# Performance work log

Hardware: AMD Instinct MI355X
Metric: run time of the kernel (lower is better)

Reference implementation:

```python
import jax, jax.numpy as jnp
import numpy as np
import math

RADIUS = 32
NUM_HEADS = 8

B, L, DIM = 2, 8192, 256


def setup_inputs() -> dict:
    key = jax.random.key(0)
    k1, k2, k3, k4, k5 = jax.random.split(key, 5)
    s_in = 1.0 / math.sqrt(DIM)
    return {
        "x": jax.random.normal(k1, (B, L, DIM), dtype=jnp.float32),
        "w_qkv": jax.random.normal(k2, (DIM, 3 * DIM), dtype=jnp.float32) * s_in,
        "b_qkv": jax.random.normal(k3, (3 * DIM,), dtype=jnp.float32) * 0.01,
        "w_proj": jax.random.normal(k4, (DIM, DIM), dtype=jnp.float32) * s_in,
        "b_proj": jax.random.normal(k5, (DIM,), dtype=jnp.float32) * 0.01,
    }


def reference(x, w_qkv, b_qkv, w_proj, b_proj):
    B, L, dim = x.shape
    H = NUM_HEADS
    hd = dim // H
    R = RADIUS
    W = 2 * R + 1
    scale = math.sqrt(hd)

    qkv = x @ w_qkv + b_qkv                      # (B, L, 3*dim)
    qkv = qkv.reshape(B, L, 3, H, hd)
    qkv = jnp.transpose(qkv, (2, 0, 3, 1, 4))    # (3, B, H, L, hd)
    q = qkv[0].reshape(B * H, L, hd)
    k = qkv[1].reshape(B * H, L, hd)
    v = qkv[2].reshape(B * H, L, hd)

    # zero-pad along sequence (matches F.pad value=0: boundary windows attend
    # to zero vectors with logit 0, included in softmax)
    k_p = jnp.pad(k, ((0, 0), (R, R), (0, 0)))   # (BH, L+2R, hd)
    v_p = jnp.pad(v, ((0, 0), (R, R), (0, 0)))

    idx = jnp.arange(L)[:, None] + jnp.arange(W)[None, :]  # (L, W)
    k_w = k_p[:, idx]                            # (BH, L, W, hd)
    v_w = v_p[:, idx]                            # (BH, L, W, hd)

    scores = jnp.einsum('bld,blwd->blw', q, k_w) / scale
    attn = jax.nn.softmax(scores, axis=-1)
    out = jnp.einsum('blw,blwd->bld', attn, v_w)  # (BH, L, hd)

    out = out.reshape(B, H, L, hd)
    out = jnp.transpose(out, (0, 2, 1, 3)).reshape(B, L, dim)
    return out @ w_proj + b_proj
```

## Files before the change

kernel.cpp:

```cpp
#include <hip/hip_runtime.h>
#include <hip/hip_bf16.h>
#include <math.h>

#define B_SZ 2
#define L_SZ 8192
#define DIM 256
#define H_N 8
#define HD 32
#define RAD 32
#define M_ROWS (B_SZ * L_SZ)

typedef __bf16 bf16x8 __attribute__((ext_vector_type(8)));
typedef __bf16 bf16x4 __attribute__((ext_vector_type(4)));
typedef short  s16x4  __attribute__((ext_vector_type(4)));
typedef float  f32x4  __attribute__((ext_vector_type(4)));

typedef const __attribute__((address_space(1))) void gvoid_t;
typedef __attribute__((address_space(3))) void lvoid_t;

static __device__ __forceinline__ f32x4 mfma16_bf16(bf16x4 a, bf16x4 b, f32x4 c) {
#if __has_builtin(__builtin_amdgcn_mfma_f32_16x16x16bf16_1k)
    return __builtin_amdgcn_mfma_f32_16x16x16bf16_1k(
        __builtin_bit_cast(s16x4, a), __builtin_bit_cast(s16x4, b), c, 0, 0, 0);
#elif __has_builtin(__builtin_amdgcn_mfma_f32_16x16x16_bf16)
    return __builtin_amdgcn_mfma_f32_16x16x16_bf16(a, b, c, 0, 0, 0);
#else
    f32x4 d = c;
    asm volatile("v_mfma_f32_16x16x16_bf16 %0, %1, %2, %0\n\ts_nop 7\n\ts_nop 7"
                 : "+v"(d) : "v"(a), "v"(b));
    return d;
#endif
}

__global__ __launch_bounds__(256) void prep(const float* __restrict__ wq,
                                            const float* __restrict__ wp,
                                            __bf16* __restrict__ wqT,
                                            __bf16* __restrict__ wpT) {
    int idx = blockIdx.x * 256 + threadIdx.x;
    const int N2 = 3 * DIM * DIM;
    if (idx < N2) {
        int n = idx >> 8, k = idx & 255;
        wqT[idx] = (__bf16)wq[(size_t)k * (3 * DIM) + n];
    } else {
        int i3 = idx - N2;
        int n = i3 >> 8, k = i3 & 255;
        wpT[i3] = (__bf16)wp[(size_t)k * DIM + n];
    }
}

template<int BM, int BN, int WM, int WN, int N_DIM, int K_DIM, bool OUT_BF16, bool CAST_A>
__global__ __launch_bounds__(256) void gemm_bt(const void* __restrict__ Aptr,
                                               const __bf16* __restrict__ BT,
                                               const float* __restrict__ bias,
                                               void* __restrict__ Cout) {
    constexpr int BK = 32;
    constexpr int FM = BM / WM / 16;
    constexpr int FN = BN / WN / 16;
    __shared__ __bf16 As[BM * BK];
    __shared__ __bf16 Bs[BN * BK];
    const int tid = threadIdx.x;
    const int lane = tid & 63;
    const int wave = tid >> 6;
    const int wr = wave / WN;
    const int wc = wave % WN;
    const int row0 = blockIdx.y * BM;
    const int col0 = blockIdx.x * BN;

    f32x4 acc[FM][FN] = {};

    const int fr = lane & 15;
    const int fg = lane >> 4;

    for (int k0 = 0; k0 < K_DIM; k0 += BK) {
        #pragma unroll
        for (int i = 0; i < BN / 64; ++i) {
            int c  = tid + i * 256;
            int r  = c >> 2;
            int kk = (c & 3) * 8;
            __builtin_amdgcn_global_load_lds(
                (gvoid_t*)(BT + (size_t)(col0 + r) * K_DIM + (k0 + kk)),
                (lvoid_t*)(Bs + c * 8), 16, 0, 0);
        }
        if (CAST_A) {
            const float* Af = (const float*)Aptr;
            #pragma unroll
            for (int i = 0; i < BM / 64; ++i) {
                int c  = tid + i * 256;
                int r  = c >> 2;
                int kk = (c & 3) * 8;
                const float* ap = Af + (size_t)(row0 + r) * K_DIM + (k0 + kk);
                float4 v0 = *reinterpret_cast<const float4*>(ap);
                float4 v1 = *reinterpret_cast<const float4*>(ap + 4);
                bf16x8 w;
                w[0] = (__bf16)v0.x; w[1] = (__bf16)v0.y; w[2] = (__bf16)v0.z; w[3] = (__bf16)v0.w;
                w[4] = (__bf16)v1.x; w[5] = (__bf16)v1.y; w[6] = (__bf16)v1.z; w[7] = (__bf16)v1.w;
                *reinterpret_cast<bf16x8*>(As + c * 8) = w;
            }
        } else {
            const __bf16* Ab = (const __bf16*)Aptr;
            #pragma unroll
            for (int i = 0; i < BM / 64; ++i) {
                int c  = tid + i * 256;
                int r  = c >> 2;
                int kk = (c & 3) * 8;
                __builtin_amdgcn_global_load_lds(
                    (gvoid_t*)(Ab + (size_t)(row0 + r) * K_DIM + (k0 + kk)),
                    (lvoid_t*)(As + c * 8), 16, 0, 0);
            }
        }
        asm volatile("s_waitcnt vmcnt(0)" ::: "memory");
        __syncthreads();

        bf16x8 a[FM], b[FN];
        #pragma unroll
        for (int i = 0; i < FM; ++i)
            a[i] = *reinterpret_cast<const bf16x8*>(&As[(wr * (BM / WM) + i * 16 + fr) * BK + fg * 8]);
        #pragma unroll
        for (int j = 0; j < FN; ++j)
            b[j] = *reinterpret_cast<const bf16x8*>(&Bs[(wc * (BN / WN) + j * 16 + fr) * BK + fg * 8]);
        #pragma unroll
        for (int i = 0; i < FM; ++i)
            #pragma unroll
            for (int j = 0; j < FN; ++j)
                acc[i][j] = __builtin_amdgcn_mfma_f32_16x16x32_bf16(a[i], b[j], acc[i][j], 0, 0, 0);
        __syncthreads();
    }

    #pragma unroll
    for (int i = 0; i < FM; ++i) {
        #pragma unroll
        for (int j = 0; j < FN; ++j) {
            int cc = col0 + wc * (BN / WN) + j * 16 + fr;
            float bv = bias[cc];
            #pragma unroll
            for (int r = 0; r < 4; ++r) {
                int rr = row0 + wr * (BM / WM) + i * 16 + fg * 4 + r;
                float v = acc[i][j][r] + bv;
                if (OUT_BF16)
                    ((__bf16*)Cout)[(size_t)rr * N_DIM + cc] = (__bf16)v;
                else
                    ((float*)Cout)[(size_t)rr * N_DIM + cc] = v;
            }
        }
    }
}

__global__ __launch_bounds__(256) void natt_mfma(const __bf16* __restrict__ qkv,
                                                 __bf16* __restrict__ attn_out) {
    constexpr int VS = 216;
    __shared__ __bf16 vsT[32 * VS];

    const int tid  = threadIdx.x;
    const int lane = tid & 63;
    const int wave = tid >> 6;
    const int l15  = lane & 15;
    const int fg   = lane >> 4;
    const int bh = blockIdx.y;
    const int b  = bh >> 3;
    const int h  = bh & 7;
    const int bq0 = blockIdx.x * 128;
    const int wq0 = bq0 + wave * 32;

    const __bf16* base = qkv + (size_t)b * L_SZ * 768 + h * 32;

    #pragma unroll
    for (int i = 0; i < 3; ++i) {
        int c  = tid + i * 256;
        int sp = c >> 2;
        int dq = c & 3;
        int kp = bq0 - 32 + sp;
        bf16x8 v = {};
        if (kp >= 0 && kp < L_SZ)
            v = *reinterpret_cast<const bf16x8*>(base + (size_t)kp * 768 + 512 + dq * 8);
        int g = (sp >> 3) ^ dq;
        #pragma unroll
        for (int j = 0; j < 8; ++j)
            vsT[(dq * 8 + j) * VS + g * 8 + (sp & 7)] = v[j];
    }

    bf16x8 kf[6];
    #pragma unroll
    for (int t = 0; t < 6; ++t) {
        int kp = wq0 - 32 + t * 16 + l15;
        bf16x8 kv = {};
        if (kp >= 0 && kp < L_SZ)
            kv = *reinterpret_cast<const bf16x8*>(base + (size_t)kp * 768 + 256 + fg * 8);
        kf[t] = kv;
    }
    bf16x8 qf[2];
    #pragma unroll
    for (int s = 0; s < 2; ++s)
        qf[s] = *reinterpret_cast<const bf16x8*>(base + (size_t)(wq0 + s * 16 + l15) * 768 + fg * 8);

    __syncthreads();

    const float rscale = 0.17677669529663687f;

    #pragma unroll
    for (int s = 0; s < 2; ++s) {
        f32x4 st[5];
        __builtin_amdgcn_s_setprio(1);
        #pragma unroll
        for (int t = 0; t < 5; ++t)
            st[t] = __builtin_amdgcn_mfma_f32_16x16x32_bf16(kf[s + t], qf[s], f32x4{}, 0, 0, 0);
        __builtin_amdgcn_s_setprio(0);

        const int qr = l15;
        float sum = 0.f;
        #pragma unroll
        for (int t = 0; t < 5; ++t) {
            #pragma unroll
            for (int r = 0; r < 4; ++r) {
                int pr = 16 * t + 4 * fg + r;
                bool valid = (pr >= qr) && (pr <= qr + 64);
                float e = valid ? __expf(st[t][r] * rscale) : 0.f;
                st[t][r] = e;
                sum += e;
            }
        }
        sum += __shfl_xor(sum, 16);
        sum += __shfl_xor(sum, 32);
        float inv = 1.f / sum;

        bf16x4 pf[5];
        #pragma unroll
        for (int t = 0; t < 5; ++t) {
            bf16x4 p;
            #pragma unroll
            for (int r = 0; r < 4; ++r) p[r] = (__bf16)(st[t][r] * inv);
            pf[t] = p;
        }

        f32x4 acc[2] = {};
        __builtin_amdgcn_s_setprio(1);
        #pragma unroll
        for (int c = 0; c < 5; ++c) {
            #pragma unroll
            for (int dt = 0; dt < 2; ++dt) {
                int g = (4 * wave + 2 * s + 2 * c + (fg >> 1)) ^ (2 * dt + (l15 >> 3));
                bf16x4 vf = *reinterpret_cast<const bf16x4*>(
                    &vsT[(dt * 16 + l15) * VS + g * 8 + 4 * (fg & 1)]);
                acc[dt] = mfma16_bf16(pf[c], vf, acc[dt]);
            }
        }
        __builtin_amdgcn_s_setprio(0);

        __bf16* outp = attn_out + ((size_t)(b * L_SZ + wq0 + s * 16)) * 256 + h * 32;
        #pragma unroll
        for (int dt = 0; dt < 2; ++dt)
            #pragma unroll
            for (int r = 0; r < 4; ++r)
                outp[(size_t)(fg * 4 + r) * 256 + dt * 16 + l15] = (__bf16)acc[dt][r];
    }
}

extern "C" void kernel_launch(void* const* d_in, const int* in_sizes, int n_in,
                              void* d_out, int out_size, void* d_ws, size_t ws_size,
                              hipStream_t stream) {
    const float* x      = (const float*)d_in[0];
    const float* w_qkv  = (const float*)d_in[1];
    const float* b_qkv  = (const float*)d_in[2];
    const float* w_proj = (const float*)d_in[3];
    const float* b_proj = (const float*)d_in[4];
    float* out = (float*)d_out;

    __bf16* wqkvT  = (__bf16*)d_ws;
    __bf16* wprojT = wqkvT + (size_t)(3 * DIM) * DIM;
    __bf16* qkvb   = wprojT + (size_t)DIM * DIM;
    __bf16* ab     = qkvb  + (size_t)M_ROWS * (3 * DIM);

    prep<<<1024, 256, 0, stream>>>(w_qkv, w_proj, wqkvT, wprojT);

    dim3 g1(3 * DIM / 128, M_ROWS / 128);
    gemm_bt<128, 128, 2, 2, 3 * DIM, DIM, true, true><<<g1, 256, 0, stream>>>(x, wqkvT, b_qkv, qkvb);

    dim3 g2(L_SZ / 128, B_SZ * H_N);
    natt_mfma<<<g2, 256, 0, stream>>>(qkvb, ab);

    dim3 g3(DIM / 128, M_ROWS / 64);
    gemm_bt<64, 128, 1, 4, DIM, DIM, false, false><<<g3, 256, 0, stream>>>(ab, wprojT, b_proj, out);
}
```

Baseline: 49.73 us.

## Pre-cast x to bf16 in prep and double-buffer GEMM LDS tiles

The prep kernel now also converts the fp32 input x to bf16 in a workspace buffer. This lets the QKV GEMM load A through async global-to-LDS copies instead of doing a per-tile fp32 load and cast in registers. The GEMM uses double-buffered shared memory, so the next K tile is fetched while MFMAs run on the current one, and one barrier per iteration is removed. The cost is an extra full pass that writes and rereads x in bf16, and twice the LDS per block, which may lower occupancy.

```diff
diff --git a/kernel.cpp b/kernel.cpp
--- a/kernel.cpp
+++ b/kernel.cpp
@@ -32,32 +32,41 @@
 #endif
 }
 
-__global__ __launch_bounds__(256) void prep(const float* __restrict__ wq,
+__global__ __launch_bounds__(256) void prep(const float* __restrict__ x,
+                                            const float* __restrict__ wq,
                                             const float* __restrict__ wp,
+                                            __bf16* __restrict__ xb,
                                             __bf16* __restrict__ wqT,
                                             __bf16* __restrict__ wpT) {
     int idx = blockIdx.x * 256 + threadIdx.x;
+    const int N1 = M_ROWS * DIM / 4;
     const int N2 = 3 * DIM * DIM;
-    if (idx < N2) {
-        int n = idx >> 8, k = idx & 255;
-        wqT[idx] = (__bf16)wq[(size_t)k * (3 * DIM) + n];
+    if (idx < N1) {
+        float4 v = reinterpret_cast<const float4*>(x)[idx];
+        __bf16* o = xb + (size_t)idx * 4;
+        o[0] = (__bf16)v.x; o[1] = (__bf16)v.y; o[2] = (__bf16)v.z; o[3] = (__bf16)v.w;
+    } else if (idx < N1 + N2) {
+        int i2 = idx - N1;
+        int n = i2 >> 8, k = i2 & 255;
+        wqT[i2] = (__bf16)wq[(size_t)k * (3 * DIM) + n];
     } else {
-        int i3 = idx - N2;
+        int i3 = idx - N1 - N2;
         int n = i3 >> 8, k = i3 & 255;
         wpT[i3] = (__bf16)wp[(size_t)k * DIM + n];
     }
 }
 
-template<int BM, int BN, int WM, int WN, int N_DIM, int K_DIM, bool OUT_BF16, bool CAST_A>
-__global__ __launch_bounds__(256) void gemm_bt(const void* __restrict__ Aptr,
+template<int BM, int BN, int WM, int WN, int N_DIM, int K_DIM, bool OUT_BF16>
+__global__ __launch_bounds__(256) void gemm_bt(const __bf16* __restrict__ A,
                                                const __bf16* __restrict__ BT,
                                                const float* __restrict__ bias,
                                                void* __restrict__ Cout) {
     constexpr int BK = 32;
     constexpr int FM = BM / WM / 16;
     constexpr int FN = BN / WN / 16;
-    __shared__ __bf16 As[BM * BK];
-    __shared__ __bf16 Bs[BN * BK];
+    constexpr int NT = K_DIM / BK;
+    __shared__ __bf16 As[2][BM * BK];
+    __shared__ __bf16 Bs[2][BN * BK];
     const int tid = threadIdx.x;
     const int lane = tid & 63;
     const int wave = tid >> 6;
@@ -71,7 +80,16 @@
     const int fr = lane & 15;
     const int fg = lane >> 4;
 
-    for (int k0 = 0; k0 < K_DIM; k0 += BK) {
+    auto stage = [&](int buf, int k0) {
+        #pragma unroll
+        for (int i = 0; i < BM / 64; ++i) {
+            int c  = tid + i * 256;
+            int r  = c >> 2;
+            int kk = (c & 3) * 8;
+            __builtin_amdgcn_global_load_lds(
+                (gvoid_t*)(A + (size_t)(row0 + r) * K_DIM + (k0 + kk)),
+                (lvoid_t*)(&As[buf][c * 8]), 16, 0, 0);
+        }
         #pragma unroll
         for (int i = 0; i < BN / 64; ++i) {
             int c  = tid + i * 256;
@@ -79,52 +97,36 @@
             int kk = (c & 3) * 8;
             __builtin_amdgcn_global_load_lds(
                 (gvoid_t*)(BT + (size_t)(col0 + r) * K_DIM + (k0 + kk)),
-                (lvoid_t*)(Bs + c * 8), 16, 0, 0);
-        }
-        if (CAST_A) {
-            const float* Af = (const float*)Aptr;
-            #pragma unroll
-            for (int i = 0; i < BM / 64; ++i) {
-                int c  = tid + i * 256;
-                int r  = c >> 2;
-                int kk = (c & 3) * 8;
-                const float* ap = Af + (size_t)(row0 + r) * K_DIM + (k0 + kk);
-                float4 v0 = *reinterpret_cast<const float4*>(ap);
-                float4 v1 = *reinterpret_cast<const float4*>(ap + 4);
-                bf16x8 w;
-                w[0] = (__bf16)v0.x; w[1] = (__bf16)v0.y; w[2] = (__bf16)v0.z; w[3] = (__bf16)v0.w;
-                w[4] = (__bf16)v1.x; w[5] = (__bf16)v1.y; w[6] = (__bf16)v1.z; w[7] = (__bf16)v1.w;
-                *reinterpret_cast<bf16x8*>(As + c * 8) = w;
-            }
-        } else {
-            const __bf16* Ab = (const __bf16*)Aptr;
-            #pragma unroll
-            for (int i = 0; i < BM / 64; ++i) {
-                int c  = tid + i * 256;
-                int r  = c >> 2;
-                int kk = (c & 3) * 8;
-                __builtin_amdgcn_global_load_lds(
-                    (gvoid_t*)(Ab + (size_t)(row0 + r) * K_DIM + (k0 + kk)),
-                    (lvoid_t*)(As + c * 8), 16, 0, 0);
-            }
-        }
+                (lvoid_t*)(&Bs[buf][c * 8]), 16, 0, 0);
+        }
+    };
+    auto compute = [&](int buf) {
+        bf16x8 a[FM], b[FN];
+        #pragma unroll
+        for (int i = 0; i < FM; ++i)
+            a[i] = *reinterpret_cast<const bf16x8*>(&As[buf][(wr * (BM / WM) + i * 16 + fr) * BK + fg * 8]);
+        #pragma unroll
+        for (int j = 0; j < FN; ++j)
+            b[j] = *reinterpret_cast<const bf16x8*>(&Bs[buf][(wc * (BN / WN) + j * 16 + fr) * BK + fg * 8]);
+        #pragma unroll
+        for (int i = 0; i < FM; ++i)
+            #pragma unroll
+            for (int j = 0; j < FN; ++j)
+                acc[i][j] = __builtin_amdgcn_mfma_f32_16x16x32_bf16(a[i], b[j], acc[i][j], 0, 0, 0);
+    };
+
+    stage(0, 0);
+    asm volatile("s_waitcnt vmcnt(0)" ::: "memory");
+    __syncthreads();
+    int cur = 0;
+    for (int t = 0; t < NT - 1; ++t) {
+        stage(cur ^ 1, (t + 1) * BK);
+        compute(cur);
         asm volatile("s_waitcnt vmcnt(0)" ::: "memory");
         __syncthreads();
-
-        bf16x8 a[FM], b[FN];
-        #pragma unroll
-        for (int i = 0; i < FM; ++i)
-            a[i] = *reinterpret_cast<const bf16x8*>(&As[(wr * (BM / WM) + i * 16 + fr) * BK + fg * 8]);
-        #pragma unroll
-        for (int j = 0; j < FN; ++j)
-            b[j] = *reinterpret_cast<const bf16x8*>(&Bs[(wc * (BN / WN) + j * 16 + fr) * BK + fg * 8]);
-        #pragma unroll
-        for (int i = 0; i < FM; ++i)
-            #pragma unroll
-            for (int j = 0; j < FN; ++j)
-                acc[i][j] = __builtin_amdgcn_mfma_f32_16x16x32_bf16(a[i], b[j], acc[i][j], 0, 0, 0);
-        __syncthreads();
-    }
+        cur ^= 1;
+    }
+    compute(cur);
 
     #pragma unroll
     for (int i = 0; i < FM; ++i) {
@@ -264,19 +266,20 @@
     const float* b_proj = (const float*)d_in[4];
     float* out = (float*)d_out;
 
-    __bf16* wqkvT  = (__bf16*)d_ws;
+    __bf16* xb     = (__bf16*)d_ws;
+    __bf16* wqkvT  = xb    + (size_t)M_ROWS * DIM;
     __bf16* wprojT = wqkvT + (size_t)(3 * DIM) * DIM;
     __bf16* qkvb   = wprojT + (size_t)DIM * DIM;
     __bf16* ab     = qkvb  + (size_t)M_ROWS * (3 * DIM);
 
-    prep<<<1024, 256, 0, stream>>>(w_qkv, w_proj, wqkvT, wprojT);
+    prep<<<5120, 256, 0, stream>>>(x, w_qkv, w_proj, xb, wqkvT, wprojT);
 
     dim3 g1(3 * DIM / 128, M_ROWS / 128);
-    gemm_bt<128, 128, 2, 2, 3 * DIM, DIM, true, true><<<g1, 256, 0, stream>>>(x, wqkvT, b_qkv, qkvb);
+    gemm_bt<128, 128, 2, 2, 3 * DIM, DIM, true><<<g1, 256, 0, stream>>>(xb, wqkvT, b_qkv, qkvb);
 
     dim3 g2(L_SZ / 128, B_SZ * H_N);
     natt_mfma<<<g2, 256, 0, stream>>>(qkvb, ab);
 
     dim3 g3(DIM / 128, M_ROWS / 64);
-    gemm_bt<64, 128, 1, 4, DIM, DIM, false, false><<<g3, 256, 0, stream>>>(ab, wprojT, b_proj, out);
-}
+    gemm_bt<64, 128, 1, 4, DIM, DIM, false><<<g3, 256, 0, stream>>>(ab, wprojT, b_proj, out);
+}
```

Result: faster. 47.62 us (-4.2%).
